# Optimization experiments

Measured on AMD Instinct MI355X. Metric: run time of the kernel, lower is better.

## Reference

```python
import jax, jax.numpy as jnp
import numpy as np

BLUR = 0.01
SQRT2 = np.sqrt(2.0).astype(np.float32)


def setup_inputs() -> dict:
    key = jax.random.key(0)
    ks = jax.random.split(key, 6)
    B, N, M, DF = 4, 4096, 4096, 16
    src = jax.random.normal(ks[0], (B, N, 3), dtype=jnp.float32)
    tgt = jax.random.normal(ks[1], (B, M, 3), dtype=jnp.float32)
    # small feature scale so C_ij / (2*blur^2) stays in a numerically sane range
    src_fea = jax.random.normal(ks[2], (B, N, DF), dtype=jnp.float32) * 0.01
    tgt_fea = jax.random.normal(ks[3], (B, M, DF), dtype=jnp.float32) * 0.01
    # dual potentials from the (opaque) Sinkhorn solve; O(blur^2) so F/blur^2 ~ O(1)
    F_i = jax.random.normal(ks[4], (B, N), dtype=jnp.float32) * (BLUR ** 2)
    G_j = jax.random.normal(ks[5], (B, M), dtype=jnp.float32) * (BLUR ** 2)
    return {"src": src, "tgt": tgt, "src_fea": src_fea, "tgt_fea": tgt_fea,
            "F_i": F_i, "G_j": G_j}


def _solve_rigid(x, y, w):
    # x: BxNxD points, y: BxNxD mapped points, w: BxNx1 weights
    B, N, D = x.shape
    sum_w = jnp.sum(w, axis=1, keepdims=True)                 # Bx1x1
    mu_x = jnp.sum(x * w, axis=1, keepdims=True) / sum_w      # Bx1xD
    mu_y = jnp.sum(y * w, axis=1, keepdims=True) / sum_w
    wx_hat = (x - mu_x) * w
    wy_hat = (y - mu_y) * w
    a = jnp.einsum('bnd,bne->bde', wy_hat, wx_hat)            # BxDxD = wy^T @ wx
    u, s, vh = jnp.linalg.svd(a)                              # a = u @ diag(s) @ vh
    v = jnp.swapaxes(vh, -1, -2)                              # torch.svd's V
    det = jnp.linalg.det(u @ v)                               # (B,)
    c = jnp.ones((B, D), dtype=x.dtype).at[:, -1].set(det)
    r = (u * c[:, :, None]) @ vh                              # (u*c) @ v^T
    t = mu_y - jnp.swapaxes(r @ jnp.swapaxes(mu_x, 1, 2), 1, 2)
    return r, t.reshape(B, D)


def reference(src, tgt, src_fea, tgt_fea, F_i, G_j):
    # weights are all ones -> log(a_i)=log(b_j)=0, weight1 divide is a no-op
    inv = 1.0 / (SQRT2 * BLUR)
    xx = src_fea * inv                                        # BxNxDf
    yy = tgt_fea * inv                                        # BxMxDf
    f_i = F_i / (BLUR ** 2)                                   # BxN
    g_j = G_j / (BLUR ** 2)                                   # BxM
    # C_ij = ||xx_i - yy_j||^2 via expansion
    x2 = jnp.sum(xx * xx, axis=-1)                            # BxN
    y2 = jnp.sum(yy * yy, axis=-1)                            # BxM
    xy = jnp.einsum('bnd,bmd->bnm', xx, yy)                   # BxNxM
    log_P = (f_i - x2)[:, :, None] + (g_j - y2)[:, None, :] + 2.0 * xy
    lse = jax.nn.logsumexp(log_P, axis=2)                     # BxN
    P_norm = jnp.exp(log_P - lse[:, :, None])                 # softmax over M
    mapped_position = jnp.einsum('bnm,bmd->bnd', P_norm, tgt) # sumsoftmaxweight
    mapped_mass_ratio = jnp.exp(lse)[:, :, None]              # exp(logP).sum(2)/1
    rotation, trans = _solve_rigid(src, mapped_position, mapped_mass_ratio)
    return rotation, trans
```

## Files before the change

### kernel.cpp

```cpp
#include <hip/hip_runtime.h>
#include <hip/hip_bf16.h>
#include <math.h>

#define BB 4
#define NN 4096
#define MM 4096
#define JC 16
#define CHUNK (MM / JC)
#define TPC (CHUNK / 32)

#define INVF  70.71067811865475f
#define IB2   10000.0f
#define INV2  5000.0f
#define LOG2E 1.4426950408889634f
#define SCY   (INVF * 2.0f * LOG2E)

#define YF_F   0
#define TG4_F  262144
#define PART_F 327680
#define BLK_F  (PART_F + BB * JC * NN * 4)

typedef __attribute__((ext_vector_type(2)))  float f32x2;
typedef __attribute__((ext_vector_type(8)))  short short8v;
typedef __attribute__((ext_vector_type(16))) float f32x16;

static __device__ __forceinline__ unsigned short f2bf(float x) {
  unsigned int u = __builtin_bit_cast(unsigned int, x);
  u += 0x7fffu + ((u >> 16) & 1u);
  return (unsigned short)(u >> 16);
}
static __device__ __forceinline__ float bf2f(unsigned short h) {
  unsigned int u = ((unsigned int)h) << 16;
  return __builtin_bit_cast(float, u);
}
static __device__ __forceinline__ void splitbf(float v, unsigned short& h, unsigned short& l) {
  h = f2bf(v);
  l = f2bf(v - bf2f(h));
}
static __device__ __forceinline__ f32x2 pkfma(f32x2 a, f32x2 b, f32x2 c) {
  f32x2 d;
  asm("v_pk_fma_f32 %0, %1, %2, %3" : "=v"(d) : "v"(a), "v"(b), "v"(c));
  return d;
}

__global__ __launch_bounds__(256) void prep_kernel(
    const float* __restrict__ tgt_fea, const float* __restrict__ G_j,
    const float* __restrict__ tgt, float* __restrict__ ws) {
  int idx = blockIdx.x * 256 + threadIdx.x;
  int b = idx >> 12, j = idx & (MM - 1);
  const float4* tf = (const float4*)(tgt_fea + (size_t)idx * 16);
  float f[16];
  float ss = 0.f;
  #pragma unroll
  for (int k = 0; k < 4; ++k) {
    float4 v = tf[k];
    f[4*k+0] = v.x; f[4*k+1] = v.y; f[4*k+2] = v.z; f[4*k+3] = v.w;
    ss += v.x*v.x + v.y*v.y + v.z*v.z + v.w*v.w;
  }
  float y2n = ss * INV2;

  unsigned short vh[16], vl[16];
  #pragma unroll
  for (int k = 0; k < 16; ++k) splitbf(f[k] * SCY, vh[k], vl[k]);

  uint4* base = (uint4*)(ws + YF_F) + ((size_t)b * (MM/32) + (j >> 5)) * 128;
  int ll = j & 31, lh = 32 + (j & 31);
  base[0*64 + ll] = make_uint4(
      (unsigned)vh[0] | ((unsigned)vh[1] << 16), (unsigned)vh[2] | ((unsigned)vh[3] << 16),
      (unsigned)vh[8] | ((unsigned)vh[9] << 16), (unsigned)vh[10] | ((unsigned)vh[11] << 16));
  base[1*64 + ll] = make_uint4(
      (unsigned)vl[0] | ((unsigned)vl[1] << 16), (unsigned)vl[2] | ((unsigned)vl[3] << 16),
      (unsigned)vl[8] | ((unsigned)vl[9] << 16), (unsigned)vl[10] | ((unsigned)vl[11] << 16));
  base[0*64 + lh] = make_uint4(
      (unsigned)vh[4] | ((unsigned)vh[5] << 16), (unsigned)vh[6] | ((unsigned)vh[7] << 16),
      (unsigned)vh[12] | ((unsigned)vh[13] << 16), (unsigned)vh[14] | ((unsigned)vh[15] << 16));
  base[1*64 + lh] = make_uint4(
      (unsigned)vl[4] | ((unsigned)vl[5] << 16), (unsigned)vl[6] | ((unsigned)vl[7] << 16),
      (unsigned)vl[12] | ((unsigned)vl[13] << 16), (unsigned)vl[14] | ((unsigned)vl[15] << 16));

  float gyl = LOG2E * (G_j[idx] * IB2 - y2n);
  ((float4*)(ws + TG4_F))[idx] = make_float4(
      tgt[(size_t)idx*3+0], tgt[(size_t)idx*3+1], tgt[(size_t)idx*3+2], gyl);
}

__global__ __launch_bounds__(256, 4) void attn_kernel(
    const float* __restrict__ src_fea, const float* __restrict__ ws,
    float* __restrict__ partial) {
  __shared__ uint4  sY[TPC * 128];
  __shared__ float4 tg4s[CHUNK];
  int tid = threadIdx.x;
  int w = tid >> 6, l = tid & 63;
  int il = l & 31, h = l >> 5;
  int b = blockIdx.z, jc = blockIdx.y;

  {
    const uint4* gY = (const uint4*)(ws + YF_F)
                    + ((size_t)b * (MM/32) + jc * TPC) * 128;
    #pragma unroll
    for (int k = 0; k < TPC * 128 / 256; ++k)
      sY[tid + k * 256] = gY[tid + k * 256];
    tg4s[tid] = ((const float4*)(ws + TG4_F))[(size_t)b * MM + jc * CHUNK + tid];
  }

  int i0 = blockIdx.x * 256 + w * 64;
  union U { uint4 q; short8v s; };
  U xaH, xaL, xbH, xbL;
  #pragma unroll
  for (int t = 0; t < 2; ++t) {
    const float* sf = src_fea + ((size_t)b * NN + i0 + t * 32 + il) * 16;
    float xv[16];
    #pragma unroll
    for (int k = 0; k < 4; ++k) {
      float4 v = *(const float4*)(sf + 4 * k);
      xv[4*k+0] = v.x * INVF; xv[4*k+1] = v.y * INVF;
      xv[4*k+2] = v.z * INVF; xv[4*k+3] = v.w * INVF;
    }
    unsigned short qh[8], ql[8];
    #pragma unroll
    for (int kk = 0; kk < 4; ++kk) {
      splitbf(xv[4*h + kk],     qh[kk],   ql[kk]);
      splitbf(xv[8 + 4*h + kk], qh[4+kk], ql[4+kk]);
    }
    uint4 UH = make_uint4((unsigned)qh[0] | ((unsigned)qh[1] << 16),
                          (unsigned)qh[2] | ((unsigned)qh[3] << 16),
                          (unsigned)qh[4] | ((unsigned)qh[5] << 16),
                          (unsigned)qh[6] | ((unsigned)qh[7] << 16));
    uint4 UL = make_uint4((unsigned)ql[0] | ((unsigned)ql[1] << 16),
                          (unsigned)ql[2] | ((unsigned)ql[3] << 16),
                          (unsigned)ql[4] | ((unsigned)ql[5] << 16),
                          (unsigned)ql[6] | ((unsigned)ql[7] << 16));
    if (t == 0) { xaH.q = UH; xaL.q = UL; } else { xbH.q = UH; xbL.q = UL; }
  }

  __syncthreads();

  f32x2 t01a = {0.f,0.f}, t2sa = {0.f,0.f};
  f32x2 t01b = {0.f,0.f}, t2sb = {0.f,0.f};

  #pragma unroll 2
  for (int jt = 0; jt < TPC; ++jt) {
    U yH, yL;
    yH.q = sY[jt * 128 + l];
    yL.q = sY[jt * 128 + 64 + l];
    f32x16 z = {};
    f32x16 c1a = __builtin_amdgcn_mfma_f32_32x32x16_bf16(yL.s, xaH.s, z, 0, 0, 0);
    c1a = __builtin_amdgcn_mfma_f32_32x32x16_bf16(yH.s, xaL.s, c1a, 0, 0, 0);
    c1a = __builtin_amdgcn_mfma_f32_32x32x16_bf16(yH.s, xaH.s, c1a, 0, 0, 0);
    f32x16 c1b = __builtin_amdgcn_mfma_f32_32x32x16_bf16(yL.s, xbH.s, z, 0, 0, 0);
    c1b = __builtin_amdgcn_mfma_f32_32x32x16_bf16(yH.s, xbL.s, c1b, 0, 0, 0);
    c1b = __builtin_amdgcn_mfma_f32_32x32x16_bf16(yH.s, xbH.s, c1b, 0, 0, 0);

    #pragma unroll
    for (int r = 0; r < 16; ++r) {
      int jl = (r & 3) + 8 * (r >> 2) + (h << 2) + jt * 32;
      float4 tg = tg4s[jl];
      float pa = __builtin_amdgcn_exp2f(c1a[r] + tg.w);
      float pb = __builtin_amdgcn_exp2f(c1b[r] + tg.w);
      f32x2 pa2 = (f32x2){pa, pa}, pb2 = (f32x2){pb, pb};
      f32x2 txy = (f32x2){tg.x, tg.y}, tz1 = (f32x2){tg.z, 1.f};
      t01a = pkfma(pa2, txy, t01a); t2sa = pkfma(pa2, tz1, t2sa);
      t01b = pkfma(pb2, txy, t01b); t2sb = pkfma(pb2, tz1, t2sb);
    }
  }

  t01a.x += __shfl_xor(t01a.x, 32, 64); t01a.y += __shfl_xor(t01a.y, 32, 64);
  t2sa.x += __shfl_xor(t2sa.x, 32, 64); t2sa.y += __shfl_xor(t2sa.y, 32, 64);
  t01b.x += __shfl_xor(t01b.x, 32, 64); t01b.y += __shfl_xor(t01b.y, 32, 64);
  t2sb.x += __shfl_xor(t2sb.x, 32, 64); t2sb.y += __shfl_xor(t2sb.y, 32, 64);

  if (h == 0) {
    float4* pp = (float4*)partial + (size_t)(b * JC + jc) * NN;
    pp[i0 + il]      = make_float4(t01a.x, t01a.y, t2sa.x, t2sa.y);
    pp[i0 + 32 + il] = make_float4(t01b.x, t01b.y, t2sb.x, t2sb.y);
  }
}

__global__ __launch_bounds__(256) void combine_kernel(
    const float* __restrict__ partial, const float* __restrict__ src_fea,
    const float* __restrict__ src, const float* __restrict__ F_i,
    double* __restrict__ blockpart) {
  int b = blockIdx.x, xb = blockIdx.y, tid = threadIdx.x;
  int i = xb * 256 + tid;
  int g = b * NN + i;

  float S = 0.f, T0 = 0.f, T1 = 0.f, T2 = 0.f;
  #pragma unroll
  for (int c = 0; c < JC; ++c) {
    float4 v = ((const float4*)partial)[(size_t)(b * JC + c) * NN + i];
    T0 += v.x; T1 += v.y; T2 += v.z; S += v.w;
  }
  float invS = 1.f / S;
  float y0 = T0 * invS, y1 = T1 * invS, y2 = T2 * invS;

  const float4* sfp = (const float4*)src_fea + (size_t)g * 4;
  float ss = 0.f;
  #pragma unroll
  for (int k = 0; k < 4; ++k) {
    float4 a = sfp[k];
    ss += a.x*a.x + a.y*a.y + a.z*a.z + a.w*a.w;
  }
  float x2 = ss * INV2;
  float w = __builtin_amdgcn_exp2f((F_i[g] * IB2 - x2) * LOG2E
                                   + __builtin_amdgcn_logf(S));

  float px = src[(size_t)g * 3 + 0];
  float py = src[(size_t)g * 3 + 1];
  float pz = src[(size_t)g * 3 + 2];

  double acc[23];
  double wd = (double)w, w2 = wd * wd;
  acc[0]  = wd;
  acc[1]  = wd * px;  acc[2]  = wd * py;  acc[3]  = wd * pz;
  acc[4]  = wd * y0;  acc[5]  = wd * y1;  acc[6]  = wd * y2;
  acc[7]  = w2;
  acc[8]  = w2 * px;  acc[9]  = w2 * py;  acc[10] = w2 * pz;
  acc[11] = w2 * y0;  acc[12] = w2 * y1;  acc[13] = w2 * y2;
  acc[14] = w2 * y0 * px; acc[15] = w2 * y0 * py; acc[16] = w2 * y0 * pz;
  acc[17] = w2 * y1 * px; acc[18] = w2 * y1 * py; acc[19] = w2 * y1 * pz;
  acc[20] = w2 * y2 * px; acc[21] = w2 * y2 * py; acc[22] = w2 * y2 * pz;

  #pragma unroll
  for (int k = 0; k < 23; ++k) {
    #pragma unroll
    for (int off = 32; off > 0; off >>= 1)
      acc[k] += __shfl_down(acc[k], off, 64);
  }
  __shared__ double red[4][23];
  int wave = tid >> 6, lane = tid & 63;
  if (lane == 0) {
    #pragma unroll
    for (int k = 0; k < 23; ++k) red[wave][k] = acc[k];
  }
  __syncthreads();
  if (tid < 23) {
    double s = red[0][tid] + red[1][tid] + red[2][tid] + red[3][tid];
    blockpart[((size_t)b * 16 + xb) * 23 + tid] = s;
  }
}

__device__ __forceinline__ double det3(const double M[3][3]) {
  return M[0][0] * (M[1][1] * M[2][2] - M[1][2] * M[2][1])
       - M[0][1] * (M[1][0] * M[2][2] - M[1][2] * M[2][0])
       + M[0][2] * (M[1][0] * M[2][1] - M[1][1] * M[2][0]);
}

__global__ void finalize_kernel(const double* __restrict__ blockpart,
                                float* __restrict__ out) {
  __shared__ double sm[BB][23];
  int tid = threadIdx.x;
  int b = tid >> 6, lane = tid & 63;
  if (lane < 23) {
    double s = 0.0;
    for (int xb = 0; xb < 16; ++xb)
      s += blockpart[((size_t)b * 16 + xb) * 23 + lane];
    sm[b][lane] = s;
  }
  __syncthreads();
  if (lane != 0) return;

  double mo[23];
  #pragma unroll
  for (int k = 0; k < 23; ++k) mo[k] = sm[b][k];

  double sw = mo[0];
  double mux[3] = { mo[1] / sw, mo[2] / sw, mo[3] / sw };
  double muy[3] = { mo[4] / sw, mo[5] / sw, mo[6] / sw };
  double sw2 = mo[7];
  double A[3][3];
  for (int d = 0; d < 3; ++d)
    for (int e = 0; e < 3; ++e)
      A[d][e] = mo[14 + d * 3 + e] - muy[d] * mo[8 + e] - mux[e] * mo[11 + d]
              + sw2 * muy[d] * mux[e];

  double ATA[3][3];
  for (int p = 0; p < 3; ++p)
    for (int q = 0; q < 3; ++q)
      ATA[p][q] = A[0][p] * A[0][q] + A[1][p] * A[1][q] + A[2][p] * A[2][q];

  double V[3][3] = { {1,0,0}, {0,1,0}, {0,0,1} };
  for (int sweep = 0; sweep < 8; ++sweep) {
    for (int pair = 0; pair < 3; ++pair) {
      int p = (pair == 2) ? 1 : 0;
      int q = (pair == 0) ? 1 : 2;
      double apq = ATA[p][q];
      if (fabs(apq) < 1e-300) continue;
      double tau = (ATA[q][q] - ATA[p][p]) / (2.0 * apq);
      double tt = ((tau >= 0.0) ? 1.0 : -1.0) / (fabs(tau) + sqrt(1.0 + tau * tau));
      double c = 1.0 / sqrt(1.0 + tt * tt), sn = tt * c;
      for (int k = 0; k < 3; ++k) {
        double akp = ATA[k][p], akq = ATA[k][q];
        ATA[k][p] = c * akp - sn * akq;
        ATA[k][q] = sn * akp + c * akq;
      }
      for (int k = 0; k < 3; ++k) {
        double apk = ATA[p][k], aqk = ATA[q][k];
        ATA[p][k] = c * apk - sn * aqk;
        ATA[q][k] = sn * apk + c * aqk;
      }
      for (int k = 0; k < 3; ++k) {
        double vkp = V[k][p], vkq = V[k][q];
        V[k][p] = c * vkp - sn * vkq;
        V[k][q] = sn * vkp + c * vkq;
      }
    }
  }

  double U[3][3];
  for (int k = 0; k < 3; ++k) {
    double sv = sqrt(fmax(ATA[k][k], 0.0));
    double u0 = A[0][0] * V[0][k] + A[0][1] * V[1][k] + A[0][2] * V[2][k];
    double u1 = A[1][0] * V[0][k] + A[1][1] * V[1][k] + A[1][2] * V[2][k];
    double u2 = A[2][0] * V[0][k] + A[2][1] * V[1][k] + A[2][2] * V[2][k];
    double inv = (sv > 1e-300) ? 1.0 / sv : 0.0;
    U[0][k] = u0 * inv; U[1][k] = u1 * inv; U[2][k] = u2 * inv;
  }

  double dd = det3(U) * det3(V);
  double R[3][3];
  for (int d = 0; d < 3; ++d)
    for (int e = 0; e < 3; ++e)
      R[d][e] = U[d][0] * V[e][0] + U[d][1] * V[e][1] + U[d][2] * V[e][2];
  R[2][0] *= dd; R[2][1] *= dd; R[2][2] *= dd;

  double tr[3];
  for (int d = 0; d < 3; ++d)
    tr[d] = muy[d] - (R[d][0] * mux[0] + R[d][1] * mux[1] + R[d][2] * mux[2]);

  for (int d = 0; d < 3; ++d)
    for (int e = 0; e < 3; ++e)
      out[b * 9 + d * 3 + e] = (float)R[d][e];
  out[BB * 9 + b * 3 + 0] = (float)tr[0];
  out[BB * 9 + b * 3 + 1] = (float)tr[1];
  out[BB * 9 + b * 3 + 2] = (float)tr[2];
}

extern "C" void kernel_launch(void* const* d_in, const int* in_sizes, int n_in,
                              void* d_out, int out_size, void* d_ws, size_t ws_size,
                              hipStream_t stream) {
  const float* src     = (const float*)d_in[0];
  const float* tgt     = (const float*)d_in[1];
  const float* src_fea = (const float*)d_in[2];
  const float* tgt_fea = (const float*)d_in[3];
  const float* F_i     = (const float*)d_in[4];
  const float* G_j     = (const float*)d_in[5];
  float* ws  = (float*)d_ws;
  float* out = (float*)d_out;
  double* blockpart = (double*)(ws + BLK_F);

  prep_kernel<<<BB * MM / 256, 256, 0, stream>>>(tgt_fea, G_j, tgt, ws);
  dim3 grid(NN / 256, JC, BB);
  attn_kernel<<<grid, 256, 0, stream>>>(src_fea, ws, ws + PART_F);
  dim3 cgrid(BB, NN / 256);
  combine_kernel<<<cgrid, 256, 0, stream>>>(ws + PART_F, src_fea, src, F_i, blockpart);
  finalize_kernel<<<1, 256, 0, stream>>>(blockpart, out);
}
```

Baseline: 114.9 us.

## Fuse target prep into attention kernel and finalize into combine via last-block counter

```diff
diff --git a/kernel.cpp b/kernel.cpp
--- a/kernel.cpp
+++ b/kernel.cpp
@@ -15,10 +15,9 @@
 #define LOG2E 1.4426950408889634f
 #define SCY   (INVF * 2.0f * LOG2E)
 
-#define YF_F   0
-#define TG4_F  262144
-#define PART_F 327680
-#define BLK_F  (PART_F + BB * JC * NN * 4)
+#define PART_F 0
+#define BLK_F  (BB * JC * NN * 4)
+#define CNT_F  (BLK_F + 2944)
 
 typedef __attribute__((ext_vector_type(2)))  float f32x2;
 typedef __attribute__((ext_vector_type(8)))  short short8v;
@@ -43,49 +42,10 @@
   return d;
 }
 
-__global__ __launch_bounds__(256) void prep_kernel(
-    const float* __restrict__ tgt_fea, const float* __restrict__ G_j,
-    const float* __restrict__ tgt, float* __restrict__ ws) {
-  int idx = blockIdx.x * 256 + threadIdx.x;
-  int b = idx >> 12, j = idx & (MM - 1);
-  const float4* tf = (const float4*)(tgt_fea + (size_t)idx * 16);
-  float f[16];
-  float ss = 0.f;
-  #pragma unroll
-  for (int k = 0; k < 4; ++k) {
-    float4 v = tf[k];
-    f[4*k+0] = v.x; f[4*k+1] = v.y; f[4*k+2] = v.z; f[4*k+3] = v.w;
-    ss += v.x*v.x + v.y*v.y + v.z*v.z + v.w*v.w;
-  }
-  float y2n = ss * INV2;
-
-  unsigned short vh[16], vl[16];
-  #pragma unroll
-  for (int k = 0; k < 16; ++k) splitbf(f[k] * SCY, vh[k], vl[k]);
-
-  uint4* base = (uint4*)(ws + YF_F) + ((size_t)b * (MM/32) + (j >> 5)) * 128;
-  int ll = j & 31, lh = 32 + (j & 31);
-  base[0*64 + ll] = make_uint4(
-      (unsigned)vh[0] | ((unsigned)vh[1] << 16), (unsigned)vh[2] | ((unsigned)vh[3] << 16),
-      (unsigned)vh[8] | ((unsigned)vh[9] << 16), (unsigned)vh[10] | ((unsigned)vh[11] << 16));
-  base[1*64 + ll] = make_uint4(
-      (unsigned)vl[0] | ((unsigned)vl[1] << 16), (unsigned)vl[2] | ((unsigned)vl[3] << 16),
-      (unsigned)vl[8] | ((unsigned)vl[9] << 16), (unsigned)vl[10] | ((unsigned)vl[11] << 16));
-  base[0*64 + lh] = make_uint4(
-      (unsigned)vh[4] | ((unsigned)vh[5] << 16), (unsigned)vh[6] | ((unsigned)vh[7] << 16),
-      (unsigned)vh[12] | ((unsigned)vh[13] << 16), (unsigned)vh[14] | ((unsigned)vh[15] << 16));
-  base[1*64 + lh] = make_uint4(
-      (unsigned)vl[4] | ((unsigned)vl[5] << 16), (unsigned)vl[6] | ((unsigned)vl[7] << 16),
-      (unsigned)vl[12] | ((unsigned)vl[13] << 16), (unsigned)vl[14] | ((unsigned)vl[15] << 16));
-
-  float gyl = LOG2E * (G_j[idx] * IB2 - y2n);
-  ((float4*)(ws + TG4_F))[idx] = make_float4(
-      tgt[(size_t)idx*3+0], tgt[(size_t)idx*3+1], tgt[(size_t)idx*3+2], gyl);
-}
-
 __global__ __launch_bounds__(256, 4) void attn_kernel(
-    const float* __restrict__ src_fea, const float* __restrict__ ws,
-    float* __restrict__ partial) {
+    const float* __restrict__ src_fea, const float* __restrict__ tgt_fea,
+    const float* __restrict__ G_j, const float* __restrict__ tgt,
+    float* __restrict__ partial, unsigned int* __restrict__ counter) {
   __shared__ uint4  sY[TPC * 128];
   __shared__ float4 tg4s[CHUNK];
   int tid = threadIdx.x;
@@ -93,13 +53,45 @@
   int il = l & 31, h = l >> 5;
   int b = blockIdx.z, jc = blockIdx.y;
 
+  if (blockIdx.x == 0 && jc == 0 && b == 0 && tid == 0)
+    *counter = 0;
+
   {
-    const uint4* gY = (const uint4*)(ws + YF_F)
-                    + ((size_t)b * (MM/32) + jc * TPC) * 128;
-    #pragma unroll
-    for (int k = 0; k < TPC * 128 / 256; ++k)
-      sY[tid + k * 256] = gY[tid + k * 256];
-    tg4s[tid] = ((const float4*)(ws + TG4_F))[(size_t)b * MM + jc * CHUNK + tid];
+    int jl = tid;
+    int jg = b * MM + jc * CHUNK + jl;
+    const float4* tf = (const float4*)(tgt_fea + (size_t)jg * 16);
+    float f[16];
+    float ss = 0.f;
+    #pragma unroll
+    for (int k = 0; k < 4; ++k) {
+      float4 v = tf[k];
+      f[4*k+0] = v.x; f[4*k+1] = v.y; f[4*k+2] = v.z; f[4*k+3] = v.w;
+      ss += v.x*v.x + v.y*v.y + v.z*v.z + v.w*v.w;
+    }
+    float y2n = ss * INV2;
+
+    unsigned short vh[16], vl[16];
+    #pragma unroll
+    for (int k = 0; k < 16; ++k) splitbf(f[k] * SCY, vh[k], vl[k]);
+
+    uint4* base = &sY[(jl >> 5) * 128];
+    int ll = jl & 31, lh = 32 + (jl & 31);
+    base[0*64 + ll] = make_uint4(
+        (unsigned)vh[0] | ((unsigned)vh[1] << 16), (unsigned)vh[2] | ((unsigned)vh[3] << 16),
+        (unsigned)vh[8] | ((unsigned)vh[9] << 16), (unsigned)vh[10] | ((unsigned)vh[11] << 16));
+    base[1*64 + ll] = make_uint4(
+        (unsigned)vl[0] | ((unsigned)vl[1] << 16), (unsigned)vl[2] | ((unsigned)vl[3] << 16),
+        (unsigned)vl[8] | ((unsigned)vl[9] << 16), (unsigned)vl[10] | ((unsigned)vl[11] << 16));
+    base[0*64 + lh] = make_uint4(
+        (unsigned)vh[4] | ((unsigned)vh[5] << 16), (unsigned)vh[6] | ((unsigned)vh[7] << 16),
+        (unsigned)vh[12] | ((unsigned)vh[13] << 16), (unsigned)vh[14] | ((unsigned)vh[15] << 16));
+    base[1*64 + lh] = make_uint4(
+        (unsigned)vl[4] | ((unsigned)vl[5] << 16), (unsigned)vl[6] | ((unsigned)vl[7] << 16),
+        (unsigned)vl[12] | ((unsigned)vl[13] << 16), (unsigned)vl[14] | ((unsigned)vl[15] << 16));
+
+    float gyl = LOG2E * (G_j[jg] * IB2 - y2n);
+    tg4s[jl] = make_float4(tgt[(size_t)jg*3+0], tgt[(size_t)jg*3+1],
+                           tgt[(size_t)jg*3+2], gyl);
   }
 
   int i0 = blockIdx.x * 256 + w * 64;
@@ -152,8 +144,8 @@
 
     #pragma unroll
     for (int r = 0; r < 16; ++r) {
-      int jl = (r & 3) + 8 * (r >> 2) + (h << 2) + jt * 32;
-      float4 tg = tg4s[jl];
+      int jl2 = (r & 3) + 8 * (r >> 2) + (h << 2) + jt * 32;
+      float4 tg = tg4s[jl2];
       float pa = __builtin_amdgcn_exp2f(c1a[r] + tg.w);
       float pb = __builtin_amdgcn_exp2f(c1b[r] + tg.w);
       f32x2 pa2 = (f32x2){pa, pa}, pb2 = (f32x2){pb, pb};
@@ -175,10 +167,17 @@
   }
 }
 
+__device__ __forceinline__ double det3(const double M[3][3]) {
+  return M[0][0] * (M[1][1] * M[2][2] - M[1][2] * M[2][1])
+       - M[0][1] * (M[1][0] * M[2][2] - M[1][2] * M[2][0])
+       + M[0][2] * (M[1][0] * M[2][1] - M[1][1] * M[2][0]);
+}
+
 __global__ __launch_bounds__(256) void combine_kernel(
     const float* __restrict__ partial, const float* __restrict__ src_fea,
     const float* __restrict__ src, const float* __restrict__ F_i,
-    double* __restrict__ blockpart) {
+    double* __restrict__ blockpart, unsigned int* __restrict__ counter,
+    float* __restrict__ out) {
   int b = blockIdx.x, xb = blockIdx.y, tid = threadIdx.x;
   int i = xb * 256 + tid;
   int g = b * NN + i;
@@ -236,31 +235,32 @@
     double s = red[0][tid] + red[1][tid] + red[2][tid] + red[3][tid];
     blockpart[((size_t)b * 16 + xb) * 23 + tid] = s;
   }
-}
-
-__device__ __forceinline__ double det3(const double M[3][3]) {
-  return M[0][0] * (M[1][1] * M[2][2] - M[1][2] * M[2][1])
-       - M[0][1] * (M[1][0] * M[2][2] - M[1][2] * M[2][0])
-       + M[0][2] * (M[1][0] * M[2][1] - M[1][1] * M[2][0]);
-}
-
-__global__ void finalize_kernel(const double* __restrict__ blockpart,
-                                float* __restrict__ out) {
+
+  __threadfence();
+  __shared__ int isLast;
+  __syncthreads();
+  if (tid == 0) {
+    unsigned int old = atomicAdd(counter, 1u);
+    isLast = (old == BB * 16 - 1);
+  }
+  __syncthreads();
+  if (!isLast) return;
+  __threadfence();
+
   __shared__ double sm[BB][23];
-  int tid = threadIdx.x;
-  int b = tid >> 6, lane = tid & 63;
-  if (lane < 23) {
+  int b2 = tid >> 6, lane2 = tid & 63;
+  if (b2 < BB && lane2 < 23) {
     double s = 0.0;
-    for (int xb = 0; xb < 16; ++xb)
-      s += blockpart[((size_t)b * 16 + xb) * 23 + lane];
-    sm[b][lane] = s;
-  }
-  __syncthreads();
-  if (lane != 0) return;
+    for (int xb2 = 0; xb2 < 16; ++xb2)
+      s += blockpart[((size_t)b2 * 16 + xb2) * 23 + lane2];
+    sm[b2][lane2] = s;
+  }
+  __syncthreads();
+  if (lane2 != 0 || b2 >= BB) return;
 
   double mo[23];
   #pragma unroll
-  for (int k = 0; k < 23; ++k) mo[k] = sm[b][k];
+  for (int k = 0; k < 23; ++k) mo[k] = sm[b2][k];
 
   double sw = mo[0];
   double mux[3] = { mo[1] / sw, mo[2] / sw, mo[3] / sw };
@@ -305,21 +305,21 @@
     }
   }
 
-  double U[3][3];
+  double Umat[3][3];
   for (int k = 0; k < 3; ++k) {
     double sv = sqrt(fmax(ATA[k][k], 0.0));
     double u0 = A[0][0] * V[0][k] + A[0][1] * V[1][k] + A[0][2] * V[2][k];
     double u1 = A[1][0] * V[0][k] + A[1][1] * V[1][k] + A[1][2] * V[2][k];
     double u2 = A[2][0] * V[0][k] + A[2][1] * V[1][k] + A[2][2] * V[2][k];
     double inv = (sv > 1e-300) ? 1.0 / sv : 0.0;
-    U[0][k] = u0 * inv; U[1][k] = u1 * inv; U[2][k] = u2 * inv;
-  }
-
-  double dd = det3(U) * det3(V);
+    Umat[0][k] = u0 * inv; Umat[1][k] = u1 * inv; Umat[2][k] = u2 * inv;
+  }
+
+  double dd = det3(Umat) * det3(V);
   double R[3][3];
   for (int d = 0; d < 3; ++d)
     for (int e = 0; e < 3; ++e)
-      R[d][e] = U[d][0] * V[e][0] + U[d][1] * V[e][1] + U[d][2] * V[e][2];
+      R[d][e] = Umat[d][0] * V[e][0] + Umat[d][1] * V[e][1] + Umat[d][2] * V[e][2];
   R[2][0] *= dd; R[2][1] *= dd; R[2][2] *= dd;
 
   double tr[3];
@@ -328,10 +328,10 @@
 
   for (int d = 0; d < 3; ++d)
     for (int e = 0; e < 3; ++e)
-      out[b * 9 + d * 3 + e] = (float)R[d][e];
-  out[BB * 9 + b * 3 + 0] = (float)tr[0];
-  out[BB * 9 + b * 3 + 1] = (float)tr[1];
-  out[BB * 9 + b * 3 + 2] = (float)tr[2];
+      out[b2 * 9 + d * 3 + e] = (float)R[d][e];
+  out[BB * 9 + b2 * 3 + 0] = (float)tr[0];
+  out[BB * 9 + b2 * 3 + 1] = (float)tr[1];
+  out[BB * 9 + b2 * 3 + 2] = (float)tr[2];
 }
 
 extern "C" void kernel_launch(void* const* d_in, const int* in_sizes, int n_in,
@@ -346,11 +346,12 @@
   float* ws  = (float*)d_ws;
   float* out = (float*)d_out;
   double* blockpart = (double*)(ws + BLK_F);
-
-  prep_kernel<<<BB * MM / 256, 256, 0, stream>>>(tgt_fea, G_j, tgt, ws);
+  unsigned int* counter = (unsigned int*)(ws + CNT_F);
+
   dim3 grid(NN / 256, JC, BB);
-  attn_kernel<<<grid, 256, 0, stream>>>(src_fea, ws, ws + PART_F);
+  attn_kernel<<<grid, 256, 0, stream>>>(src_fea, tgt_fea, G_j, tgt,
+                                        ws + PART_F, counter);
   dim3 cgrid(BB, NN / 256);
-  combine_kernel<<<cgrid, 256, 0, stream>>>(ws + PART_F, src_fea, src, F_i, blockpart);
-  finalize_kernel<<<1, 256, 0, stream>>>(blockpart, out);
-}
+  combine_kernel<<<cgrid, 256, 0, stream>>>(ws + PART_F, src_fea, src, F_i,
+                                            blockpart, counter, out);
+}
```

Result: slower. 118.3 us (+3.0%).
